# Optimization experiments

Hardware: AMD Instinct MI355X
Metric: run time of the kernel (lower is better)

## Reference

```python
import jax, jax.numpy as jnp
import numpy as np

SIGMA_E, SIGMA_I, K_E, K_I = 0.6, 1.2, 0.8, 1.0
PM_STEPS, DT, BETA = 4, 0.15, 1.0
EPS = 1e-4


def setup_inputs() -> dict:
    key = jax.random.key(0)
    ks = jax.random.split(key, 12)
    B, d_in, d_lat, ch, d_out, n_c = 4096, 784, 8, 32, 10, 16
    inp = {
        "x": jax.random.normal(ks[0], (B, d_in), dtype=jnp.float32),
        "W1": jax.random.normal(ks[1], (d_in, 128), dtype=jnp.float32) * 0.03,
        "b1": jnp.zeros((128,), jnp.float32),
        "W2": jax.random.normal(ks[2], (128, d_lat), dtype=jnp.float32) * 0.08,
        "b2": jnp.zeros((d_lat,), jnp.float32),
        "centers": jax.random.normal(ks[3], (n_c, d_lat), dtype=jnp.float32) * 0.7,
        "mus": jnp.ones((n_c,), jnp.float32) * 0.5,
        "Wp": jax.random.normal(ks[4], (d_lat, ch), dtype=jnp.float32) * 0.3,
        "bp": jnp.zeros((ch,), jnp.float32),
        "Wr": jax.random.normal(ks[5], (ch, d_out), dtype=jnp.float32) * 0.15,
        "br": jnp.zeros((d_out,), jnp.float32),
        "T": 5,
    }
    return inp


def grad_ln_n(z, centers, mus):
    # z: [B,d], centers: [C,d], mus: [C]
    rvec = z[:, None, :] - centers[None, :, :]          # [B,C,d]
    r = jnp.sqrt(jnp.sum(rvec * rvec, axis=-1) + EPS)   # [B,C]
    n = 1.0 + jnp.sum(mus[None, :] / r, axis=1)          # [B]
    g = -jnp.sum((mus[None, :] / (r ** 3))[:, :, None] * rvec, axis=1)  # [B,d]
    return g / n[:, None]


def pm_field(z, centers, mus):
    for _ in range(PM_STEPS):
        z = jnp.clip(z + DT * BETA * grad_ln_n(z, centers, mus), -3.0, 3.0)
    return z


def lateral_kernel(z):
    # squared pairwise distances via the norm trick (avoids [B,B,d])
    sq = jnp.sum(z * z, axis=1)
    dist2 = jnp.maximum(sq[:, None] + sq[None, :] - 2.0 * (z @ z.T), 0.0)
    K = K_E * jnp.exp(-dist2 / (2.0 * SIGMA_E ** 2)) - K_I * jnp.exp(-dist2 / (2.0 * SIGMA_I ** 2))
    return jax.lax.stop_gradient(K)  # torch.no_grad in original


def reference(x, W1, b1, W2, b2, centers, mus, Wp, bp, Wr, br, T):
    B = x.shape[0]
    z = jnp.tanh(x.reshape(B, -1) @ W1 + b1) @ W2 + b2   # encoder
    h = jnp.zeros((B, Wr.shape[0]), x.dtype)
    for _ in range(T):
        z = pm_field(z, centers, mus)
        h = 0.9 * h + 0.1 * jnp.tanh(z @ Wp + bp)
        h = h + 0.05 * (lateral_kernel(z) @ h)
        y = h @ Wr + br
    return y
```

## Files before the change

kernel.cpp:

```cpp
#include <hip/hip_runtime.h>
#include <math.h>

#define NB    4096
#define DIN   784
#define DH    128
#define DL    8
#define NC    16
#define NCH   32
#define DO    10
#define TSTEPS 5

#define KH_ROWS   128
#define KH_TILE   64
#define KH_JSLICE 256
#define KH_P      (NB / KH_JSLICE)
#define ENC_G     7


__global__ __launch_bounds__(256) void enc1_kernel(const float* __restrict__ x,
    const float* __restrict__ W1, double* __restrict__ P)
{
    __shared__ float xsT[56][18];
    __shared__ float wss[56][128];
    const int tid = threadIdx.x;
    const int m0 = blockIdx.x * 16;
    const int kbeg = blockIdx.y * 112;
    const int cg = tid & 31, rg = tid >> 5;
    const int c0 = cg << 2, r0 = rg << 1;
    double acc[2][4] = {};
    for (int it = 0; it < 2; ++it) {
        const int k0 = kbeg + it * 56;
        __syncthreads();
        if (tid < 224) {
            int row = tid / 14, f = tid % 14;
            float4 v = *(const float4*)(x + (m0 + row) * DIN + k0 + f * 4);
            int kk = f * 4;
            xsT[kk][row] = v.x; xsT[kk + 1][row] = v.y;
            xsT[kk + 2][row] = v.z; xsT[kk + 3][row] = v.w;
        }
        for (int l = tid; l < 56 * 32; l += 256) {
            int kk = l >> 5, c = (l & 31) << 2;
            *(float4*)&wss[kk][c] = *(const float4*)(W1 + (k0 + kk) * DH + c);
        }
        __syncthreads();
#pragma unroll 8
        for (int kk = 0; kk < 56; ++kk) {
            const float2 xv = *(const float2*)&xsT[kk][r0];
            const float4 wv = *(const float4*)&wss[kk][c0];
            const double x0 = (double)xv.x, x1 = (double)xv.y;
            const double w0 = (double)wv.x, w1 = (double)wv.y;
            const double w2v = (double)wv.z, w3 = (double)wv.w;
            acc[0][0] += x0 * w0; acc[0][1] += x0 * w1;
            acc[0][2] += x0 * w2v; acc[0][3] += x0 * w3;
            acc[1][0] += x1 * w0; acc[1][1] += x1 * w1;
            acc[1][2] += x1 * w2v; acc[1][3] += x1 * w3;
        }
    }
    double* Pr = P + (size_t)blockIdx.y * (NB * DH);
#pragma unroll
    for (int i = 0; i < 2; ++i) {
        double* dst = Pr + (m0 + r0 + i) * DH + c0;
        *(double2*)dst       = make_double2(acc[i][0], acc[i][1]);
        *(double2*)(dst + 2) = make_double2(acc[i][2], acc[i][3]);
    }
}

__global__ __launch_bounds__(256) void enc2_kernel(const double* __restrict__ P,
    const float* __restrict__ b1, const float* __restrict__ W2,
    const float* __restrict__ b2, double* __restrict__ zbuf)
{
    __shared__ double As[16][132];
    __shared__ double W2d[DH * DL];
    const int tid = threadIdx.x;
    const int m0 = blockIdx.x * 16;
    for (int l = tid; l < DH * DL; l += 256) W2d[l] = (double)W2[l];
    for (int l = tid; l < 16 * 128; l += 256) {
        int row = l >> 7, k = l & 127;
        double v = (double)b1[k];
#pragma unroll
        for (int s = 0; s < ENC_G; ++s)
            v += P[(size_t)s * NB * DH + (m0 + row) * DH + k];
        As[row][k] = tanh(v);
    }
    __syncthreads();
    const int row = tid >> 4, d = (tid >> 1) & 7, half = tid & 1;
    double a = 0.0;
#pragma unroll 8
    for (int i = 0; i < 64; ++i) {
        const int k = half + (i << 1);
        a += As[row][k] * W2d[k * 8 + d];
    }
    a += __shfl_xor(a, 1);
    if (half == 0) zbuf[(m0 + row) * DL + d] = a + (double)b2[d];
}

__global__ __launch_bounds__(256) void enc_fused_kernel(const float* __restrict__ x,
    const float* __restrict__ W1, const float* __restrict__ b1,
    const float* __restrict__ W2, const float* __restrict__ b2,
    double* __restrict__ zbuf)
{
    __shared__ float  xsT[56][9];
    __shared__ float  wss[56][128];
    __shared__ double Asd[8][131];
    __shared__ double W2d[DH * DL];
    const int tid = threadIdx.x;
    const int m0 = blockIdx.x * 8;
    const int cg = tid & 31, rg = tid >> 5;
    const int c0 = cg << 2;
    for (int l = tid; l < DH * DL; l += 256) W2d[l] = (double)W2[l];
    double acc[4] = {};
    for (int it = 0; it < 14; ++it) {
        const int k0 = it * 56;
        __syncthreads();
        if (tid < 112) {
            int row = tid / 14, f = tid % 14;
            float4 v = *(const float4*)(x + (m0 + row) * DIN + k0 + f * 4);
            int kk = f * 4;
            xsT[kk][row] = v.x; xsT[kk + 1][row] = v.y;
            xsT[kk + 2][row] = v.z; xsT[kk + 3][row] = v.w;
        }
        for (int l = tid; l < 56 * 32; l += 256) {
            int kk = l >> 5, c = (l & 31) << 2;
            *(float4*)&wss[kk][c] = *(const float4*)(W1 + (k0 + kk) * DH + c);
        }
        __syncthreads();
#pragma unroll 8
        for (int kk = 0; kk < 56; ++kk) {
            const double xv = (double)xsT[kk][rg];
            const float4 wv = *(const float4*)&wss[kk][c0];
            acc[0] += xv * (double)wv.x;
            acc[1] += xv * (double)wv.y;
            acc[2] += xv * (double)wv.z;
            acc[3] += xv * (double)wv.w;
        }
    }
    __syncthreads();
#pragma unroll
    for (int j = 0; j < 4; ++j)
        Asd[rg][c0 + j] = tanh(acc[j] + (double)b1[c0 + j]);
    __syncthreads();
    {
        const int row = tid >> 5, d = (tid >> 2) & 7, kq = tid & 3;
        double a = 0.0;
#pragma unroll 8
        for (int i = 0; i < 32; ++i) {
            const int k = kq + (i << 2);
            a += Asd[row][k] * W2d[k * 8 + d];
        }
        a += __shfl_xor(a, 1);
        a += __shfl_xor(a, 2);
        if (kq == 0) zbuf[(m0 + row) * DL + d] = a + (double)b2[d];
    }
}

__global__ __launch_bounds__(256) void pmh_kernel(double* __restrict__ zbuf,
    const float* __restrict__ centers, const float* __restrict__ mus,
    const float* __restrict__ Wp, const float* __restrict__ bp,
    double* __restrict__ hB, float* __restrict__ zf, float* __restrict__ sqf,
    float* __restrict__ hAf, const float* __restrict__ part, int first)
{
    const int tid = threadIdx.x;
    const int lane = tid & 15;
    const int s = tid >> 4;
    const int i = blockIdx.x * 16 + s;
    double cz[8];
#pragma unroll
    for (int d = 0; d < 8; ++d) cz[d] = (double)centers[lane * DL + d];
    const double mu = (double)mus[lane];
    double z[8];
#pragma unroll
    for (int p = 0; p < 4; ++p) {
        double2 v = *(const double2*)(zbuf + i * DL + p * 2);
        z[p * 2] = v.x; z[p * 2 + 1] = v.y;
    }
#pragma unroll
    for (int st = 0; st < 4; ++st) {
        double rv[8];
        double ss = 1e-4;
#pragma unroll
        for (int d = 0; d < 8; ++d) { rv[d] = z[d] - cz[d]; ss += rv[d] * rv[d]; }
        double rinv = rsqrt(ss);
        double mr = mu * rinv;
        double n = mr;
        double mr3 = mr * (rinv * rinv);
        double g[8];
#pragma unroll
        for (int d = 0; d < 8; ++d) g[d] = -mr3 * rv[d];
#pragma unroll
        for (int m = 1; m < 16; m <<= 1) {
            n += __shfl_xor(n, m);
#pragma unroll
            for (int d = 0; d < 8; ++d) g[d] += __shfl_xor(g[d], m);
        }
        double sc = 0.15 / (1.0 + n);
#pragma unroll
        for (int d = 0; d < 8; ++d) z[d] = fmin(3.0, fmax(-3.0, z[d] + sc * g[d]));
    }
    if (lane == 0) {
        double sq = 0.0;
#pragma unroll
        for (int d = 0; d < 8; ++d) sq += z[d] * z[d];
        sqf[i] = (float)sq;
#pragma unroll
        for (int p = 0; p < 4; ++p)
            *(double2*)(zbuf + i * DL + p * 2) = make_double2(z[p * 2], z[p * 2 + 1]);
        float4 a = make_float4((float)z[0], (float)z[1], (float)z[2], (float)z[3]);
        float4 b = make_float4((float)z[4], (float)z[5], (float)z[6], (float)z[7]);
        *(float4*)(zf + i * DL)     = a;
        *(float4*)(zf + i * DL + 4) = b;
    }
#pragma unroll
    for (int cc = 0; cc < 2; ++cc) {
        const int c = lane + cc * 16;
        double a = (double)bp[c];
#pragma unroll
        for (int d = 0; d < 8; ++d) a += z[d] * (double)Wp[d * NCH + c];
        double ph = (double)tanhf((float)a);
        double prev = 0.0;
        if (!first) {
            prev = hB[i * NCH + c];
            if (part) {
                double sp = 0.0;
#pragma unroll
                for (int p = 0; p < KH_P; ++p)
                    sp += (double)part[(size_t)p * (NB * NCH) + i * NCH + c];
                prev += 0.05 * sp;
            }
        }
        double hv = 0.9 * prev + 0.1 * ph;
        hAf[i * NCH + c] = (float)hv;
        hB[i * NCH + c] = hv;
    }
}

__global__ __launch_bounds__(256) void kh_kernel(const float* __restrict__ zf,
    const float* __restrict__ sqf, const float* __restrict__ hAf,
    double* __restrict__ hB, float* __restrict__ part)
{
    __shared__ float zjs[KH_TILE][8];
    __shared__ float sqjs[KH_TILE];
    __shared__ float hs[KH_TILE][32];
    __shared__ float bufA[KH_ROWS][33];
    __shared__ float bufB[KH_ROWS][33];
    const int tid = threadIdx.x;
    const int wave = tid >> 6, lane = tid & 63;
    const int row0 = blockIdx.x * KH_ROWS + lane;
    const int j_base = blockIdx.y * KH_JSLICE;
    float zr0[8], zr1[8];
    {
        float4 a = *(const float4*)(zf + row0 * 8);
        float4 b = *(const float4*)(zf + row0 * 8 + 4);
        zr0[0] = a.x; zr0[1] = a.y; zr0[2] = a.z; zr0[3] = a.w;
        zr0[4] = b.x; zr0[5] = b.y; zr0[6] = b.z; zr0[7] = b.w;
        float4 c = *(const float4*)(zf + (row0 + 64) * 8);
        float4 d = *(const float4*)(zf + (row0 + 64) * 8 + 4);
        zr1[0] = c.x; zr1[1] = c.y; zr1[2] = c.z; zr1[3] = c.w;
        zr1[4] = d.x; zr1[5] = d.y; zr1[6] = d.z; zr1[7] = d.w;
    }
    const float sq0 = sqf[row0], sq1 = sqf[row0 + 64];
    const float invI = 1.0f / 2.88f;
    float acc0[32] = {}, acc1[32] = {};
    for (int jt = 0; jt < KH_JSLICE / KH_TILE; ++jt) {
        const int j0 = j_base + jt * KH_TILE;
        __syncthreads();
        {
            int jj = tid >> 2, p = (tid & 3) << 1;
            *(float2*)&zjs[jj][p] = *(const float2*)(zf + (j0 + jj) * 8 + p);
        }
        if (tid < KH_TILE) sqjs[tid] = sqf[j0 + tid];
        for (int l = tid; l < KH_TILE * 8; l += 256) {
            int jh = l >> 3, p = (l & 7) << 2;
            *(float4*)&hs[jh][p] = *(const float4*)(hAf + (j0 + jh) * NCH + p);
        }
        __syncthreads();
        const int jjbeg = wave * 16;
#pragma unroll 2
        for (int q = 0; q < 16; ++q) {
            const int jj = jjbeg + q;
            const float4 a = *(const float4*)&zjs[jj][0];
            const float4 b = *(const float4*)&zjs[jj][4];
            const float sqj = sqjs[jj];
            float dot0 = zr0[0] * a.x + zr0[1] * a.y + zr0[2] * a.z + zr0[3] * a.w
                       + zr0[4] * b.x + zr0[5] * b.y + zr0[6] * b.z + zr0[7] * b.w;
            float dot1 = zr1[0] * a.x + zr1[1] * a.y + zr1[2] * a.z + zr1[3] * a.w
                       + zr1[4] * b.x + zr1[5] * b.y + zr1[6] * b.z + zr1[7] * b.w;
            float d20 = fmaxf(sq0 + sqj - 2.0f * dot0, 0.0f);
            float d21 = fmaxf(sq1 + sqj - 2.0f * dot1, 0.0f);
            float e0 = __expf(-d20 * invI), e1 = __expf(-d21 * invI);
            float t0 = e0 * e0, t1 = e1 * e1;
            float K0 = 0.8f * (t0 * t0) - e0;
            float K1 = 0.8f * (t1 * t1) - e1;
#pragma unroll
            for (int c = 0; c < 32; c += 4) {
                const float4 hv = *(const float4*)&hs[jj][c];
                acc0[c]     += K0 * hv.x; acc0[c + 1] += K0 * hv.y;
                acc0[c + 2] += K0 * hv.z; acc0[c + 3] += K0 * hv.w;
                acc1[c]     += K1 * hv.x; acc1[c + 1] += K1 * hv.y;
                acc1[c + 2] += K1 * hv.z; acc1[c + 3] += K1 * hv.w;
            }
        }
    }
    __syncthreads();
    if (wave == 1) {
#pragma unroll
        for (int c = 0; c < 32; ++c) { bufA[lane][c] = acc0[c]; bufA[lane + 64][c] = acc1[c]; }
    } else if (wave == 3) {
#pragma unroll
        for (int c = 0; c < 32; ++c) { bufB[lane][c] = acc0[c]; bufB[lane + 64][c] = acc1[c]; }
    }
    __syncthreads();
    if (wave == 0) {
#pragma unroll
        for (int c = 0; c < 32; ++c) { acc0[c] += bufA[lane][c]; acc1[c] += bufA[lane + 64][c]; }
    } else if (wave == 2) {
#pragma unroll
        for (int c = 0; c < 32; ++c) { acc0[c] += bufB[lane][c]; acc1[c] += bufB[lane + 64][c]; }
    }
    __syncthreads();
    if (wave == 2) {
#pragma unroll
        for (int c = 0; c < 32; ++c) { bufA[lane][c] = acc0[c]; bufA[lane + 64][c] = acc1[c]; }
    }
    __syncthreads();
    if (wave == 0) {
#pragma unroll
        for (int c = 0; c < 32; ++c) { acc0[c] += bufA[lane][c]; acc1[c] += bufA[lane + 64][c]; }
        if (part) {
            float* p0 = part + (size_t)blockIdx.y * (NB * NCH) + row0 * NCH;
            float* p1 = p0 + 64 * NCH;
#pragma unroll
            for (int c = 0; c < 32; c += 4) {
                *(float4*)(p0 + c) = make_float4(acc0[c], acc0[c + 1], acc0[c + 2], acc0[c + 3]);
                *(float4*)(p1 + c) = make_float4(acc1[c], acc1[c + 1], acc1[c + 2], acc1[c + 3]);
            }
        } else {
#pragma unroll
            for (int c = 0; c < 32; ++c) {
                atomicAdd(&hB[row0 * NCH + c], 0.05 * (double)acc0[c]);
                atomicAdd(&hB[(row0 + 64) * NCH + c], 0.05 * (double)acc1[c]);
            }
        }
    }
}

__global__ __launch_bounds__(256) void y_kernel(const double* __restrict__ h,
    const float* __restrict__ part, const float* __restrict__ Wr,
    const float* __restrict__ br, float* __restrict__ y)
{
    __shared__ double hsy[16][33];
    __shared__ double wrs[NCH * DO];
    __shared__ double brs[DO];
    const int tid = threadIdx.x;
    const int rb = blockIdx.x * 16;
    for (int l = tid; l < 16 * 32; l += 256) {
        int row = l >> 5, k = l & 31;
        const int gi = (rb + row) * NCH + k;
        double v = h[gi];
        if (part) {
            double sp = 0.0;
#pragma unroll
            for (int p = 0; p < KH_P; ++p) sp += (double)part[(size_t)p * (NB * NCH) + gi];
            v += 0.05 * sp;
        }
        hsy[row][k] = v;
    }
    for (int l = tid; l < NCH * DO; l += 256) wrs[l] = (double)Wr[l];
    if (tid < DO) brs[tid] = (double)br[tid];
    __syncthreads();
    const int row = tid >> 4, col = tid & 15;
    if (col < DO) {
        double a = brs[col];
#pragma unroll
        for (int k = 0; k < NCH; ++k) a += hsy[row][k] * wrs[k * DO + col];
        y[(rb + row) * DO + col] = (float)a;
    }
}

extern "C" void kernel_launch(void* const* d_in, const int* in_sizes, int n_in,
                              void* d_out, int out_size, void* d_ws, size_t ws_size,
                              hipStream_t stream)
{
    const float* x   = (const float*)d_in[0];
    const float* W1  = (const float*)d_in[1];
    const float* b1  = (const float*)d_in[2];
    const float* W2  = (const float*)d_in[3];
    const float* b2  = (const float*)d_in[4];
    const float* cen = (const float*)d_in[5];
    const float* mus = (const float*)d_in[6];
    const float* Wp  = (const float*)d_in[7];
    const float* bp  = (const float*)d_in[8];
    const float* Wr  = (const float*)d_in[9];
    const float* br  = (const float*)d_in[10];

    float* y = (float*)d_out;
    double* zbuf = (double*)d_ws;
    double* hB   = zbuf + NB * DL;
    float*  zf   = (float*)(hB + NB * NCH);
    float*  sqf  = zf + NB * DL;
    float*  hAf  = sqf + NB;
    float*  part = hAf + NB * NCH;
    double* Penc = (double*)(part + (size_t)KH_P * NB * NCH);

    const size_t need_part = (size_t)(NB * DL + NB * NCH) * 8
                           + (size_t)(NB * DL + NB + NB * NCH + KH_P * NB * NCH) * 4;
    const size_t need_full = need_part + (size_t)ENC_G * NB * DH * 8;
    float* pp = (ws_size >= need_part) ? part : (float*)nullptr;

    if (ws_size >= need_full) {
        enc1_kernel<<<dim3(NB / 16, ENC_G), 256, 0, stream>>>(x, W1, Penc);
        enc2_kernel<<<NB / 16, 256, 0, stream>>>(Penc, b1, W2, b2, zbuf);
    } else {
        enc_fused_kernel<<<NB / 8, 256, 0, stream>>>(x, W1, b1, W2, b2, zbuf);
    }
    for (int t = 0; t < TSTEPS; ++t) {
        pmh_kernel<<<NB / 16, 256, 0, stream>>>(zbuf, cen, mus, Wp, bp, hB,
                                                zf, sqf, hAf, pp, t == 0 ? 1 : 0);
        kh_kernel<<<dim3(NB / KH_ROWS, KH_P), 256, 0, stream>>>(zf, sqf, hAf, hB, pp);
    }
    y_kernel<<<NB / 16, 256, 0, stream>>>(hB, pp, Wr, br, y);
}
```

Measured before the change: 353.7 us.

## Halve kh j-slice, load tile once, alias reduction buffers into one smem array

The lateral-kernel block now covers 128 columns instead of 256 and loads the whole column slice once, with a single barrier, instead of looping over four 64-column tiles. All shared buffers are packed into one aliased array, so the reduction scratch reuses the tile storage and per-block LDS drops. This doubles the grid and the number of partial slices written to and summed from global memory, and adds extra barriers to the cross-wave reduction.

Result: faster. 330.8 us (-6.5%).

```diff
diff --git a/kernel.cpp b/kernel.cpp
--- a/kernel.cpp
+++ b/kernel.cpp
@@ -11,8 +11,7 @@
 #define TSTEPS 5
 
 #define KH_ROWS   128
-#define KH_TILE   64
-#define KH_JSLICE 256
+#define KH_JSLICE 128
 #define KH_P      (NB / KH_JSLICE)
 #define ENC_G     7
 
@@ -233,19 +232,19 @@
     }
 }
 
+#define SM_Z   0
+#define SM_SQ  1024
+#define SM_H   1152
+#define SM_ALL 5248
 __global__ __launch_bounds__(256) void kh_kernel(const float* __restrict__ zf,
     const float* __restrict__ sqf, const float* __restrict__ hAf,
     double* __restrict__ hB, float* __restrict__ part)
 {
-    __shared__ float zjs[KH_TILE][8];
-    __shared__ float sqjs[KH_TILE];
-    __shared__ float hs[KH_TILE][32];
-    __shared__ float bufA[KH_ROWS][33];
-    __shared__ float bufB[KH_ROWS][33];
+    __shared__ float smem[SM_ALL];
     const int tid = threadIdx.x;
     const int wave = tid >> 6, lane = tid & 63;
     const int row0 = blockIdx.x * KH_ROWS + lane;
-    const int j_base = blockIdx.y * KH_JSLICE;
+    const int j0 = blockIdx.y * KH_JSLICE;
     float zr0[8], zr1[8];
     {
         float4 a = *(const float4*)(zf + row0 * 8);
@@ -259,72 +258,72 @@
     }
     const float sq0 = sqf[row0], sq1 = sqf[row0 + 64];
     const float invI = 1.0f / 2.88f;
+    {
+        int jj = tid >> 1, p = (tid & 1) << 2;
+        *(float4*)&smem[SM_Z + jj * 8 + p] = *(const float4*)(zf + (j0 + jj) * 8 + p);
+    }
+    if (tid < KH_JSLICE) smem[SM_SQ + tid] = sqf[j0 + tid];
+    for (int l = tid; l < KH_JSLICE * 8; l += 256) {
+        int jh = l >> 3, p = (l & 7) << 2;
+        *(float4*)&smem[SM_H + jh * 32 + p] = *(const float4*)(hAf + (j0 + jh) * NCH + p);
+    }
+    __syncthreads();
     float acc0[32] = {}, acc1[32] = {};
-    for (int jt = 0; jt < KH_JSLICE / KH_TILE; ++jt) {
-        const int j0 = j_base + jt * KH_TILE;
-        __syncthreads();
-        {
-            int jj = tid >> 2, p = (tid & 3) << 1;
-            *(float2*)&zjs[jj][p] = *(const float2*)(zf + (j0 + jj) * 8 + p);
-        }
-        if (tid < KH_TILE) sqjs[tid] = sqf[j0 + tid];
-        for (int l = tid; l < KH_TILE * 8; l += 256) {
-            int jh = l >> 3, p = (l & 7) << 2;
-            *(float4*)&hs[jh][p] = *(const float4*)(hAf + (j0 + jh) * NCH + p);
-        }
-        __syncthreads();
-        const int jjbeg = wave * 16;
+    const int jjbeg = wave * 32;
 #pragma unroll 2
-        for (int q = 0; q < 16; ++q) {
-            const int jj = jjbeg + q;
-            const float4 a = *(const float4*)&zjs[jj][0];
-            const float4 b = *(const float4*)&zjs[jj][4];
-            const float sqj = sqjs[jj];
-            float dot0 = zr0[0] * a.x + zr0[1] * a.y + zr0[2] * a.z + zr0[3] * a.w
-                       + zr0[4] * b.x + zr0[5] * b.y + zr0[6] * b.z + zr0[7] * b.w;
-            float dot1 = zr1[0] * a.x + zr1[1] * a.y + zr1[2] * a.z + zr1[3] * a.w
-                       + zr1[4] * b.x + zr1[5] * b.y + zr1[6] * b.z + zr1[7] * b.w;
-            float d20 = fmaxf(sq0 + sqj - 2.0f * dot0, 0.0f);
-            float d21 = fmaxf(sq1 + sqj - 2.0f * dot1, 0.0f);
-            float e0 = __expf(-d20 * invI), e1 = __expf(-d21 * invI);
-            float t0 = e0 * e0, t1 = e1 * e1;
-            float K0 = 0.8f * (t0 * t0) - e0;
-            float K1 = 0.8f * (t1 * t1) - e1;
-#pragma unroll
-            for (int c = 0; c < 32; c += 4) {
-                const float4 hv = *(const float4*)&hs[jj][c];
-                acc0[c]     += K0 * hv.x; acc0[c + 1] += K0 * hv.y;
-                acc0[c + 2] += K0 * hv.z; acc0[c + 3] += K0 * hv.w;
-                acc1[c]     += K1 * hv.x; acc1[c + 1] += K1 * hv.y;
-                acc1[c + 2] += K1 * hv.z; acc1[c + 3] += K1 * hv.w;
-            }
+    for (int q = 0; q < 32; ++q) {
+        const int jj = jjbeg + q;
+        const float4 a = *(const float4*)&smem[SM_Z + jj * 8];
+        const float4 b = *(const float4*)&smem[SM_Z + jj * 8 + 4];
+        const float sqj = smem[SM_SQ + jj];
+        float dot0 = zr0[0] * a.x + zr0[1] * a.y + zr0[2] * a.z + zr0[3] * a.w
+                   + zr0[4] * b.x + zr0[5] * b.y + zr0[6] * b.z + zr0[7] * b.w;
+        float dot1 = zr1[0] * a.x + zr1[1] * a.y + zr1[2] * a.z + zr1[3] * a.w
+                   + zr1[4] * b.x + zr1[5] * b.y + zr1[6] * b.z + zr1[7] * b.w;
+        float d20 = fmaxf(sq0 + sqj - 2.0f * dot0, 0.0f);
+        float d21 = fmaxf(sq1 + sqj - 2.0f * dot1, 0.0f);
+        float e0 = __expf(-d20 * invI), e1 = __expf(-d21 * invI);
+        float t0 = e0 * e0, t1 = e1 * e1;
+        float K0 = 0.8f * (t0 * t0) - e0;
+        float K1 = 0.8f * (t1 * t1) - e1;
+#pragma unroll
+        for (int c = 0; c < 32; c += 4) {
+            const float4 hv = *(const float4*)&smem[SM_H + jj * 32 + c];
+            acc0[c]     += K0 * hv.x; acc0[c + 1] += K0 * hv.y;
+            acc0[c + 2] += K0 * hv.z; acc0[c + 3] += K0 * hv.w;
+            acc1[c]     += K1 * hv.x; acc1[c + 1] += K1 * hv.y;
+            acc1[c + 2] += K1 * hv.z; acc1[c + 3] += K1 * hv.w;
         }
     }
     __syncthreads();
     if (wave == 1) {
 #pragma unroll
-        for (int c = 0; c < 32; ++c) { bufA[lane][c] = acc0[c]; bufA[lane + 64][c] = acc1[c]; }
-    } else if (wave == 3) {
-#pragma unroll
-        for (int c = 0; c < 32; ++c) { bufB[lane][c] = acc0[c]; bufB[lane + 64][c] = acc1[c]; }
+        for (int c = 0; c < 32; ++c) { smem[lane * 33 + c] = acc0[c]; smem[(lane + 64) * 33 + c] = acc1[c]; }
     }
     __syncthreads();
     if (wave == 0) {
 #pragma unroll
-        for (int c = 0; c < 32; ++c) { acc0[c] += bufA[lane][c]; acc1[c] += bufA[lane + 64][c]; }
-    } else if (wave == 2) {
-#pragma unroll
-        for (int c = 0; c < 32; ++c) { acc0[c] += bufB[lane][c]; acc1[c] += bufB[lane + 64][c]; }
+        for (int c = 0; c < 32; ++c) { acc0[c] += smem[lane * 33 + c]; acc1[c] += smem[(lane + 64) * 33 + c]; }
+    }
+    __syncthreads();
+    if (wave == 3) {
+#pragma unroll
+        for (int c = 0; c < 32; ++c) { smem[lane * 33 + c] = acc0[c]; smem[(lane + 64) * 33 + c] = acc1[c]; }
     }
     __syncthreads();
     if (wave == 2) {
 #pragma unroll
-        for (int c = 0; c < 32; ++c) { bufA[lane][c] = acc0[c]; bufA[lane + 64][c] = acc1[c]; }
+        for (int c = 0; c < 32; ++c) { acc0[c] += smem[lane * 33 + c]; acc1[c] += smem[(lane + 64) * 33 + c]; }
+    }
+    __syncthreads();
+    if (wave == 2) {
+#pragma unroll
+        for (int c = 0; c < 32; ++c) { smem[lane * 33 + c] = acc0[c]; smem[(lane + 64) * 33 + c] = acc1[c]; }
     }
     __syncthreads();
     if (wave == 0) {
 #pragma unroll
-        for (int c = 0; c < 32; ++c) { acc0[c] += bufA[lane][c]; acc1[c] += bufA[lane + 64][c]; }
+        for (int c = 0; c < 32; ++c) { acc0[c] += smem[lane * 33 + c]; acc1[c] += smem[(lane + 64) * 33 + c]; }
         if (part) {
             float* p0 = part + (size_t)blockIdx.y * (NB * NCH) + row0 * NCH;
             float* p1 = p0 + 64 * NCH;
```
